# Kernel optimization log

Measured on AMD Instinct MI355X. Metric: run time of the kernel, lower is better.

Reference implementation:

```python
import jax, jax.numpy as jnp
import numpy as np


def _pack_ternary(codes):
    # codes: [N, K] uint8 in {0,1,2} (encoded = ternary_value + 1)
    N, K = codes.shape
    c = codes.reshape(N, K // 4, 4).astype(np.uint8)
    shifts = np.array([0, 2, 4, 6], dtype=np.uint8)
    packed = (c << shifts).sum(axis=-1).astype(np.uint8)
    return packed  # [N, K//4]


def setup_inputs() -> dict:
    key = jax.random.key(0)
    k1, k2 = jax.random.split(key)
    M, K, N = 8192, 4096, 4096
    x = jax.random.normal(k1, (M, K), dtype=jnp.float16)
    # valid INT2 packed ternary weights: 2-bit fields in {0,1,2} = value+1
    codes = np.asarray(jax.random.randint(k2, (N, K), 0, 3), dtype=np.uint8)
    W_packed = jnp.asarray(_pack_ternary(codes), dtype=jnp.uint8)
    gamma = jnp.ones((1,), dtype=jnp.float32)
    return {"x": x, "W_packed": W_packed, "gamma": gamma}


def _unpack_w(W_packed, K):
    # W_packed: [N, K//4] uint8 -> ternary float32 W: [N, K]
    N = W_packed.shape[0]
    shifts = jnp.array([0, 2, 4, 6], dtype=jnp.uint8)
    fields = (W_packed[:, :, None] >> shifts) & jnp.uint8(3)  # [N, K//4, 4]
    w = fields.reshape(N, -1)[:, :K].astype(jnp.float32) - 1.0  # {-1,0,1}
    return w


def reference(x, W_packed, gamma):
    K = x.shape[-1]
    W = _unpack_w(W_packed, K)  # [N, K] ternary
    # Y = X @ W.T * gamma (kernel does fp16 TC GEMM with inline dequant scale)
    Xf = x.astype(jnp.float32)
    Y = jnp.einsum('mk,nk->mn', Xf, W) * gamma[0]
    return Y.astype(jnp.float16)
```

## Files before the change

### kernel.cpp

```cpp
#include <hip/hip_runtime.h>
#include <cstdint>
#include <cstddef>

#define M_DIM 8192
#define N_DIM 4096
#define K_DIM 4096

typedef _Float16 f16x8 __attribute__((ext_vector_type(8)));
typedef float f32x4 __attribute__((ext_vector_type(4)));
typedef unsigned short ushort8 __attribute__((ext_vector_type(8)));

#define GLOAD_LDS16(g, l)                                                      \
  __builtin_amdgcn_global_load_lds(                                            \
      (const __attribute__((address_space(1))) void*)(g),                      \
      (__attribute__((address_space(3))) void*)(l), 16, 0, 0)

__device__ inline uint32_t lutf16(uint32_t c) {
  return (c == 1u) ? 0u : (0x3C00u | ((uint32_t)(c == 0u) << 15));
}

__global__ __launch_bounds__(256) void prep_x(const float4* __restrict__ X,
                                              ushort8* __restrict__ Xf) {
  int i = blockIdx.x * 256 + threadIdx.x;
  float4 f0 = X[2 * (size_t)i], f1 = X[2 * (size_t)i + 1];
  ushort8 us;
  us[0] = __builtin_bit_cast(uint16_t, (_Float16)f0.x);
  us[1] = __builtin_bit_cast(uint16_t, (_Float16)f0.y);
  us[2] = __builtin_bit_cast(uint16_t, (_Float16)f0.z);
  us[3] = __builtin_bit_cast(uint16_t, (_Float16)f0.w);
  us[4] = __builtin_bit_cast(uint16_t, (_Float16)f1.x);
  us[5] = __builtin_bit_cast(uint16_t, (_Float16)f1.y);
  us[6] = __builtin_bit_cast(uint16_t, (_Float16)f1.z);
  us[7] = __builtin_bit_cast(uint16_t, (_Float16)f1.w);
  Xf[i] = us;
}

__global__ __launch_bounds__(256) void prep_w(const uint2* __restrict__ W,
                                              uint4* __restrict__ Wf) {
  int i = blockIdx.x * 256 + threadIdx.x;
  uint2 wv = W[(size_t)i];
  uint32_t x = wv.x & 0xFFu, y = wv.y & 0xFFu;
  uint4 o;
  o.x = lutf16(x & 3u) | (lutf16((x >> 2) & 3u) << 16);
  o.y = lutf16((x >> 4) & 3u) | (lutf16((x >> 6) & 3u) << 16);
  o.z = lutf16(y & 3u) | (lutf16((y >> 2) & 3u) << 16);
  o.w = lutf16((y >> 4) & 3u) | (lutf16((y >> 6) & 3u) << 16);
  Wf[i] = o;
}

__global__ __launch_bounds__(512, 2) void gemm8(
    const _Float16* __restrict__ A,
    const _Float16* __restrict__ B,
    const float* __restrict__ G,
    float* __restrict__ C) {
  __shared__ __align__(16) _Float16 As[2][16384];
  __shared__ __align__(16) _Float16 Bs[2][16384];

  const int tid = threadIdx.x;
  const int wid = tid >> 6;
  const int lane = tid & 63;
  const int wr = wid >> 2;
  const int wcq = wid & 3;
  const int fr = lane & 15, kg = lane >> 4;

  int bid = (int)blockIdx.x;
  int swz = ((bid & 7) << 6) | (bid >> 3);
  const int bm = (swz >> 4) * 256;
  const int bn = (swz & 15) * 256;

  const int sr8 = lane >> 3;
  const int scol = ((lane & 7) ^ sr8) * 8;

  f32x4 acc[8][4] = {};
  f16x8 bfr[4][2];
  f16x8 afr[2][2];

#define STAGE(t, ht)                                                           \
  do {                                                                         \
    const int buf_ = (t) & 1;                                                  \
    const int kt_ = (t) << 6;                                                  \
    const _Float16* src_ =                                                     \
        ((ht) < 2) ? (B + (size_t)bn * K_DIM) : (A + (size_t)bm * K_DIM);      \
    _Float16* dst_ = ((ht) < 2) ? Bs[buf_] : As[buf_];                         \
    const int h_ = (ht) & 1;                                                   \
    _Pragma("unroll") for (int j_ = 0; j_ < 2; ++j_) {                         \
      int sg_ = h_ * 16 + wid * 2 + j_;                                        \
      int row_ = sg_ * 8 + sr8;                                                \
      GLOAD_LDS16(src_ + (size_t)row_ * K_DIM + kt_ + scol, dst_ + sg_ * 512); \
    }                                                                          \
  } while (0)

#define STAGE_FULL(t)                                                          \
  do { STAGE(t, 0); STAGE(t, 1); STAGE(t, 2); STAGE(t, 3); } while (0)

#define READ_B(t)                                                              \
  do {                                                                         \
    const int buf_ = (t) & 1;                                                  \
    _Pragma("unroll") for (int ni_ = 0; ni_ < 4; ++ni_)                        \
        _Pragma("unroll") for (int ks_ = 0; ks_ < 2; ++ks_) {                  \
      int row_ = wcq * 64 + ni_ * 16 + fr;                                     \
      bfr[ni_][ks_] = *reinterpret_cast<const f16x8*>(                         \
          Bs[buf_] + row_ * 64 + (((ks_ * 4 + kg) ^ (row_ & 7)) * 8));         \
    }                                                                          \
  } while (0)

#define READ_A(t, q)                                                           \
  do {                                                                         \
    const int buf_ = (t) & 1;                                                  \
    _Pragma("unroll") for (int m2_ = 0; m2_ < 2; ++m2_)                        \
        _Pragma("unroll") for (int ks_ = 0; ks_ < 2; ++ks_) {                  \
      int row_ = wr * 128 + ((q) * 2 + m2_) * 16 + fr;                         \
      afr[m2_][ks_] = *reinterpret_cast<const f16x8*>(                         \
          As[buf_] + row_ * 64 + (((ks_ * 4 + kg) ^ (row_ & 7)) * 8));         \
    }                                                                          \
  } while (0)

#define MFMA_Q(q)                                                              \
  do {                                                                         \
    __builtin_amdgcn_s_setprio(1);                                             \
    _Pragma("unroll") for (int m2_ = 0; m2_ < 2; ++m2_)                        \
        _Pragma("unroll") for (int ni_ = 0; ni_ < 4; ++ni_)                    \
            _Pragma("unroll") for (int ks_ = 0; ks_ < 2; ++ks_)                \
                acc[(q) * 2 + m2_][ni_] =                                      \
        __builtin_amdgcn_mfma_f32_16x16x32_f16(                                \
            afr[m2_][ks_], bfr[ni_][ks_], acc[(q) * 2 + m2_][ni_], 0, 0, 0);   \
    __builtin_amdgcn_s_setprio(0);                                             \
  } while (0)

#define VM0() asm volatile("s_waitcnt vmcnt(0)" ::: "memory")

  STAGE_FULL(0);
  for (int t = 0; t < 63; ++t) {
    VM0();
    __builtin_amdgcn_s_barrier();
    STAGE_FULL(t + 1);
    READ_B(t);
    READ_A(t, 0); MFMA_Q(0);
    READ_A(t, 1); MFMA_Q(1);
    READ_A(t, 2); MFMA_Q(2);
    READ_A(t, 3); MFMA_Q(3);
  }
  VM0();
  __builtin_amdgcn_s_barrier();
  READ_B(63);
  READ_A(63, 0); MFMA_Q(0);
  READ_A(63, 1); MFMA_Q(1);
  READ_A(63, 2); MFMA_Q(2);
  READ_A(63, 3); MFMA_Q(3);

  float g = G[0];
  if (!(__builtin_fabsf(g) >= 0.001f && __builtin_fabsf(g) <= 1000.0f)) g = 1.0f;
#pragma unroll
  for (int m = 0; m < 8; ++m)
#pragma unroll
    for (int ni = 0; ni < 4; ++ni) {
      int col = bn + wcq * 64 + ni * 16 + fr;
      int row0 = bm + wr * 128 + m * 16 + kg * 4;
#pragma unroll
      for (int j = 0; j < 4; ++j)
        C[(size_t)(row0 + j) * N_DIM + col] = acc[m][ni][j] * g;
    }
#undef STAGE
#undef STAGE_FULL
#undef READ_B
#undef READ_A
#undef MFMA_Q
#undef VM0
}

__global__ __launch_bounds__(256) void gemm_inline(
    const float* __restrict__ X, const uint32_t* __restrict__ W,
    const float* __restrict__ G, float* __restrict__ C) {
  __shared__ __align__(16) _Float16 As[128 * 64];
  __shared__ __align__(16) _Float16 Bs[128 * 64];

  const int tid = threadIdx.x;
  const int wave = tid >> 6;
  const int lane = tid & 63;
  const int wr = wave >> 1, wc = wave & 1;
  const int fr = lane & 15, kg = lane >> 4;
  const int bm = blockIdx.y * 128, bn = blockIdx.x * 128;
  const int brow = tid >> 1, bhalf = tid & 1;

  f32x4 acc[4][4] = {};

  for (int kt = 0; kt < K_DIM; kt += 64) {
#pragma unroll
    for (int i = 0; i < 4; ++i) {
      int c = i * 256 + tid;
      int row = c >> 3, cc = c & 7;
      const float4* p =
          (const float4*)(X + (size_t)(bm + row) * K_DIM + kt + cc * 8);
      float4 f0 = p[0], f1 = p[1];
      ushort8 us;
      us[0] = __builtin_bit_cast(uint16_t, (_Float16)f0.x);
      us[1] = __builtin_bit_cast(uint16_t, (_Float16)f0.y);
      us[2] = __builtin_bit_cast(uint16_t, (_Float16)f0.z);
      us[3] = __builtin_bit_cast(uint16_t, (_Float16)f0.w);
      us[4] = __builtin_bit_cast(uint16_t, (_Float16)f1.x);
      us[5] = __builtin_bit_cast(uint16_t, (_Float16)f1.y);
      us[6] = __builtin_bit_cast(uint16_t, (_Float16)f1.z);
      us[7] = __builtin_bit_cast(uint16_t, (_Float16)f1.w);
      *reinterpret_cast<ushort8*>((uint16_t*)As + row * 64 +
                                  (cc ^ (row & 7)) * 8) = us;
    }
    {
      const uint32_t* wp =
          W + (size_t)(bn + brow) * 1024 + (kt >> 2) + bhalf * 8;
      uint32_t w[8];
      *(uint4*)(w) = *(const uint4*)(wp);
      *(uint4*)(w + 4) = *(const uint4*)(wp + 4);
#pragma unroll
      for (int q = 0; q < 4; ++q) {
        uint32_t x = w[2 * q] & 0xFFu, y = w[2 * q + 1] & 0xFFu;
        uint4 o;
        o.x = lutf16(x & 3u) | (lutf16((x >> 2) & 3u) << 16);
        o.y = lutf16((x >> 4) & 3u) | (lutf16((x >> 6) & 3u) << 16);
        o.z = lutf16(y & 3u) | (lutf16((y >> 2) & 3u) << 16);
        o.w = lutf16((y >> 4) & 3u) | (lutf16((y >> 6) & 3u) << 16);
        int slot = (bhalf * 4 + q) ^ (brow & 7);
        *reinterpret_cast<uint4*>((uint16_t*)Bs + brow * 64 + slot * 8) = o;
      }
    }
    __syncthreads();

#pragma unroll
    for (int ks = 0; ks < 2; ++ks) {
      f16x8 a[4], b[4];
#pragma unroll
      for (int r = 0; r < 4; ++r) {
        int row = wr * 64 + r * 16 + fr;
        a[r] = *reinterpret_cast<const f16x8*>(
            As + row * 64 + ((ks * 4 + kg) ^ (row & 7)) * 8);
      }
#pragma unroll
      for (int c = 0; c < 4; ++c) {
        int row = wc * 64 + c * 16 + fr;
        b[c] = *reinterpret_cast<const f16x8*>(
            Bs + row * 64 + ((ks * 4 + kg) ^ (row & 7)) * 8);
      }
#pragma unroll
      for (int r = 0; r < 4; ++r)
#pragma unroll
        for (int c = 0; c < 4; ++c)
          acc[r][c] = __builtin_amdgcn_mfma_f32_16x16x32_f16(a[r], b[c],
                                                             acc[r][c], 0, 0, 0);
    }
    __syncthreads();
  }

  float g = G[0];
  if (!(__builtin_fabsf(g) >= 0.001f && __builtin_fabsf(g) <= 1000.0f)) g = 1.0f;
#pragma unroll
  for (int r = 0; r < 4; ++r)
#pragma unroll
    for (int c = 0; c < 4; ++c) {
      int col = bn + wc * 64 + c * 16 + fr;
      int row0 = bm + wr * 64 + r * 16 + kg * 4;
#pragma unroll
      for (int j = 0; j < 4; ++j)
        C[(size_t)(row0 + j) * N_DIM + col] = acc[r][c][j] * g;
    }
}

extern "C" void kernel_launch(void* const* d_in, const int* in_sizes, int n_in,
                              void* d_out, int out_size, void* d_ws,
                              size_t ws_size, hipStream_t stream) {
  const float* x = (const float*)d_in[0];
  const uint32_t* w32 = (const uint32_t*)d_in[1];
  const float* gamma = (const float*)d_in[2];
  float* out = (float*)d_out;
  (void)in_sizes; (void)n_in; (void)out_size;

  const size_t xf_bytes = (size_t)M_DIM * K_DIM * 2;
  const size_t wf_bytes = (size_t)N_DIM * K_DIM * 2;

  if (ws_size >= xf_bytes + wf_bytes) {
    _Float16* xf = (_Float16*)d_ws;
    _Float16* wf = (_Float16*)((char*)d_ws + xf_bytes);
    prep_x<<<M_DIM * K_DIM / 8 / 256, 256, 0, stream>>>((const float4*)x,
                                                        (ushort8*)xf);
    prep_w<<<N_DIM * K_DIM / 8 / 256, 256, 0, stream>>>((const uint2*)w32,
                                                        (uint4*)wf);
    gemm8<<<(M_DIM / 256) * (N_DIM / 256), 512, 0, stream>>>(xf, wf, gamma,
                                                             out);
  } else {
    dim3 grid(N_DIM / 128, M_DIM / 128);
    gemm_inline<<<grid, 256, 0, stream>>>(x, w32, gamma, out);
  }
}
```

Baseline: 304.1 us.

## Interleave half-tile global-to-LDS loads with MFMA quarters using partial vmcnt waits

Replaces the per-tile full stage, wait-all, then barrier loop with a finer software pipeline. Each half-tile load (two global_load_lds per thread) is issued between MFMA quarters, and partial vmcnt(4) waits let some loads stay in flight across barriers. The loop is unrolled by two tiles and the s_setprio calls around the MFMA blocks are removed. The aim is to hide global-memory latency behind compute instead of stalling on vmcnt(0) every tile, at the cost of more barriers per tile and tighter reasoning about double-buffer hazards.

Result: no change. 298.3 us (-1.9%).

```diff
diff --git a/kernel.cpp b/kernel.cpp
--- a/kernel.cpp
+++ b/kernel.cpp
@@ -90,9 +90,6 @@
     }                                                                          \
   } while (0)
 
-#define STAGE_FULL(t)                                                          \
-  do { STAGE(t, 0); STAGE(t, 1); STAGE(t, 2); STAGE(t, 3); } while (0)
-
 #define READ_B(t)                                                              \
   do {                                                                         \
     const int buf_ = (t) & 1;                                                  \
@@ -117,35 +114,43 @@
 
 #define MFMA_Q(q)                                                              \
   do {                                                                         \
-    __builtin_amdgcn_s_setprio(1);                                             \
     _Pragma("unroll") for (int m2_ = 0; m2_ < 2; ++m2_)                        \
         _Pragma("unroll") for (int ni_ = 0; ni_ < 4; ++ni_)                    \
             _Pragma("unroll") for (int ks_ = 0; ks_ < 2; ++ks_)                \
                 acc[(q) * 2 + m2_][ni_] =                                      \
         __builtin_amdgcn_mfma_f32_16x16x32_f16(                                \
             afr[m2_][ks_], bfr[ni_][ks_], acc[(q) * 2 + m2_][ni_], 0, 0, 0);   \
-    __builtin_amdgcn_s_setprio(0);                                             \
-  } while (0)
-
+  } while (0)
+
+#define BAR() __builtin_amdgcn_s_barrier()
+#define VM4() asm volatile("s_waitcnt vmcnt(4)" ::: "memory")
 #define VM0() asm volatile("s_waitcnt vmcnt(0)" ::: "memory")
 
-  STAGE_FULL(0);
-  for (int t = 0; t < 63; ++t) {
-    VM0();
-    __builtin_amdgcn_s_barrier();
-    STAGE_FULL(t + 1);
-    READ_B(t);
-    READ_A(t, 0); MFMA_Q(0);
-    READ_A(t, 1); MFMA_Q(1);
-    READ_A(t, 2); MFMA_Q(2);
-    READ_A(t, 3); MFMA_Q(3);
+  STAGE(0, 0); STAGE(0, 1); STAGE(0, 2); STAGE(0, 3);
+  STAGE(1, 0); STAGE(1, 1);
+  VM4();
+  BAR();
+
+  for (int i = 0; i < 31; ++i) {
+    const int t = 2 * i;
+    STAGE(t + 1, 2); STAGE(t + 1, 3);
+    READ_B(t); READ_A(t, 0); MFMA_Q(0); BAR();
+    STAGE(t + 2, 0); READ_A(t, 1); MFMA_Q(1); BAR();
+    STAGE(t + 2, 1); READ_A(t, 2); MFMA_Q(2); BAR();
+    READ_A(t, 3); MFMA_Q(3); VM4(); BAR();
+    STAGE(t + 2, 2); READ_B(t + 1); READ_A(t + 1, 0); MFMA_Q(0); BAR();
+    STAGE(t + 2, 3); READ_A(t + 1, 1); MFMA_Q(1); BAR();
+    STAGE(t + 3, 0); READ_A(t + 1, 2); MFMA_Q(2); BAR();
+    STAGE(t + 3, 1); READ_A(t + 1, 3); MFMA_Q(3); VM4(); BAR();
   }
-  VM0();
-  __builtin_amdgcn_s_barrier();
-  READ_B(63);
-  READ_A(63, 0); MFMA_Q(0);
-  READ_A(63, 1); MFMA_Q(1);
-  READ_A(63, 2); MFMA_Q(2);
+  STAGE(63, 2); STAGE(63, 3);
+  READ_B(62); READ_A(62, 0); MFMA_Q(0); BAR();
+  READ_A(62, 1); MFMA_Q(1); BAR();
+  READ_A(62, 2); MFMA_Q(2); BAR();
+  READ_A(62, 3); MFMA_Q(3); VM0(); BAR();
+  READ_B(63); READ_A(63, 0); MFMA_Q(0); BAR();
+  READ_A(63, 1); MFMA_Q(1); BAR();
+  READ_A(63, 2); MFMA_Q(2); BAR();
   READ_A(63, 3); MFMA_Q(3);
 
   float g = G[0];
@@ -161,10 +166,11 @@
         C[(size_t)(row0 + j) * N_DIM + col] = acc[m][ni][j] * g;
     }
 #undef STAGE
-#undef STAGE_FULL
 #undef READ_B
 #undef READ_A
 #undef MFMA_Q
+#undef BAR
+#undef VM4
 #undef VM0
 }
 
```
